# Performance work log

Measured on AMD Instinct MI355X. Metric: run time of the kernel, lower is better.

The kernel has to match this reference:

```python
import jax, jax.numpy as jnp
import numpy as np

N, E, G = 50000, 800000, 128
IN, HID, OUT, H = 128, 64, 32, 4
EPS = 1e-5


def _bn(x, g, b, m, v):
    # BatchNorm1d in eval mode: normalize with running stats
    return (x - m) * jax.lax.rsqrt(v + EPS) * g + b


def _gat(x, src, dst, W, att_src, att_dst, bias, n):
    # PyG GATConv, concat=False: mean over heads
    h = (x @ W).reshape(n, H, -1)                      # [N,H,C]
    a_src = (h * att_src).sum(-1)                      # [N,H]
    a_dst = (h * att_dst).sum(-1)                      # [N,H]
    e = jax.nn.leaky_relu(a_src[src] + a_dst[dst], 0.2)  # [E,H]
    m = jax.ops.segment_max(e, dst, num_segments=n)    # segment softmax over incoming edges
    e = jnp.exp(e - m[dst])
    s = jax.ops.segment_sum(e, dst, num_segments=n)
    alpha = e / s[dst]                                  # [E,H]
    out = jax.ops.segment_sum(alpha[:, :, None] * h[src], dst, num_segments=n)  # [N,H,C]
    return out.mean(axis=1) + bias


def setup_inputs() -> dict:
    key = jax.random.key(0)
    ks = jax.random.split(key, 20)
    d = {
        "x": jax.random.normal(ks[0], (N, IN), jnp.float32),
        "edge_index": jax.random.randint(ks[1], (2, E), 0, N),
        "batch": jnp.sort(jax.random.randint(ks[2], (N,), 0, G)),
        # input_norm
        "in_gamma": jax.random.normal(ks[3], (IN,)) * 0.05 + 1.0,
        "in_beta": jax.random.normal(ks[4], (IN,)) * 0.05,
        "in_mean": jax.random.normal(ks[5], (IN,)) * 0.05,
        "in_var": jax.random.uniform(ks[6], (IN,)) + 0.5,
        # gat1
        "W1": jax.random.normal(ks[7], (IN, H * HID)) * (1.0 / np.sqrt(IN)),
        "as1": jax.random.normal(ks[8], (H, HID)) * 0.1,
        "ad1": jax.random.normal(ks[9], (H, HID)) * 0.1,
        "b1": jnp.zeros((HID,)),
        "bn1_g": jnp.ones((HID,)),
        "bn1_b": jnp.zeros((HID,)),
        "bn1_m": jax.random.normal(ks[10], (HID,)) * 0.05,
        "bn1_v": jax.random.uniform(ks[11], (HID,)) + 0.5,
        # gat2
        "W2": jax.random.normal(ks[12], (HID, H * HID)) * (1.0 / np.sqrt(HID)),
        "as2": jax.random.normal(ks[13], (H, HID)) * 0.1,
        "ad2": jax.random.normal(ks[14], (H, HID)) * 0.1,
        "b2": jnp.zeros((HID,)),
        "bn2_g": jnp.ones((HID,)),
        "bn2_b": jnp.zeros((HID,)),
        "bn2_m": jax.random.normal(ks[15], (HID,)) * 0.05,
        "bn2_v": jax.random.uniform(ks[16], (HID,)) + 0.5,
        # head
        "fc1_w": jax.random.normal(ks[17], (HID, HID // 2)) * (1.0 / np.sqrt(HID)),
        "fc1_b": jnp.zeros((HID // 2,)),
        "fc2_w": jax.random.normal(ks[18], (HID // 2, OUT)) * (1.0 / np.sqrt(HID // 2)),
        "fc2_b": jnp.zeros((OUT,)),
    }
    return d


def reference(x, edge_index, batch, in_gamma, in_beta, in_mean, in_var,
              W1, as1, ad1, b1, bn1_g, bn1_b, bn1_m, bn1_v,
              W2, as2, ad2, b2, bn2_g, bn2_b, bn2_m, bn2_v,
              fc1_w, fc1_b, fc2_w, fc2_b):
    n = x.shape[0]
    # PyG GATConv adds self-loops by default
    loop = jnp.arange(n)
    src = jnp.concatenate([edge_index[0], loop])
    dst = jnp.concatenate([edge_index[1], loop])

    h = _bn(x, in_gamma, in_beta, in_mean, in_var)
    h = _gat(h, src, dst, W1, as1, ad1, b1, n)
    h = jax.nn.relu(_bn(h, bn1_g, bn1_b, bn1_m, bn1_v))
    # dropout p=0.3 is identity in eval mode
    h = _gat(h, src, dst, W2, as2, ad2, b2, n)
    h = jax.nn.relu(_bn(h, bn2_g, bn2_b, bn2_m, bn2_v))

    # global mean pool over graphs
    sums = jax.ops.segment_sum(h, batch, num_segments=G)
    cnts = jax.ops.segment_sum(jnp.ones((n,), h.dtype), batch, num_segments=G)
    emb = sums / jnp.maximum(cnts, 1.0)[:, None]

    out = jax.nn.relu(emb @ fc1_w + fc1_b)
    return out @ fc2_w + fc2_b
```

## Files before the change

### kernel.cpp

```cpp
#include <hip/hip_runtime.h>
#include <hip/hip_bf16.h>

#define EPS   1e-5f
#define NH    4
#define DIN   128
#define DHID  64
#define DOUT  32
#define PNODES 256
#define CAP   128
#define GM    32
#define NBUCK 64
#define BSTR  16
#define EPT   16
#define EPB   (256 * EPT)

typedef __attribute__((ext_vector_type(8))) short short8;
typedef __attribute__((ext_vector_type(4))) float f32x4;
typedef __attribute__((ext_vector_type(2))) float f32x2;

__device__ __forceinline__ float us2f(unsigned short u) {
    return __uint_as_float((unsigned)u << 16);
}
__device__ __forceinline__ unsigned short f2us(float v) {
    __hip_bfloat16 hb = __float2bfloat16(v);
    return *(unsigned short*)&hb;
}
__device__ __forceinline__ unsigned char f2e4m3(float v) {
    int p = __builtin_amdgcn_cvt_pk_fp8_f32(v, 0.f, 0, false);
    return (unsigned char)(p & 0xff);
}
__device__ __forceinline__ float lrelu(float a) { return (a >= 0.f) ? a : 0.2f * a; }

__global__ __launch_bounds__(256) void k_setup(
    int* __restrict__ deg, float* __restrict__ pool, int* __restrict__ bcur,
    int N, int npool,
    const float* __restrict__ ing, const float* __restrict__ inb,
    const float* __restrict__ inm, const float* __restrict__ inv,
    const float* __restrict__ W1, const float* __restrict__ W2,
    const float* __restrict__ as1, const float* __restrict__ ad1,
    const float* __restrict__ as2, const float* __restrict__ ad2,
    const float* __restrict__ b1,
    const float* __restrict__ bn1g, const float* __restrict__ bn1b,
    const float* __restrict__ bn1m, const float* __restrict__ bn1v,
    unsigned short* __restrict__ Wt, unsigned short* __restrict__ Wt2,
    unsigned short* __restrict__ Wast1, unsigned short* __restrict__ Wast2,
    float* __restrict__ scl1, float* __restrict__ shf1,
    float* __restrict__ sclX, float* __restrict__ shfX)
{
    int g = blockIdx.x * blockDim.x + threadIdx.x;
    if (g < N) deg[g] = 1;
    if (g < npool) pool[g] = 0.f;
    if (g < NBUCK * BSTR) bcur[g] = 0;
    if (g < 256 * DIN) {
        int n = g >> 7, k = g & 127;
        Wt[g] = f2us(W1[(size_t)k * 256 + n]);
    }
    if (g < 256 * DHID) {
        int n = g >> 6, k = g & 63;
        Wt2[g] = f2us(W2[(size_t)k * 256 + n]);
    }
    if (g < 16 * DIN) {
        int c = g >> 7, k = g & 127;
        float s = 0.f;
        if (c < 4)      { for (int j = 0; j < 64; ++j) s += W1[(size_t)k * 256 + c * 64 + j] * as1[c * 64 + j]; }
        else if (c < 8) { for (int j = 0; j < 64; ++j) s += W1[(size_t)k * 256 + (c - 4) * 64 + j] * ad1[(c - 4) * 64 + j]; }
        Wast1[g] = f2us(s);
    }
    if (g < 16 * DHID) {
        int c = g >> 6, k = g & 63;
        float s = 0.f;
        if (c < 4)      { for (int j = 0; j < 64; ++j) s += W2[(size_t)k * 256 + c * 64 + j] * as2[c * 64 + j]; }
        else if (c < 8) { for (int j = 0; j < 64; ++j) s += W2[(size_t)k * 256 + (c - 4) * 64 + j] * ad2[(c - 4) * 64 + j]; }
        Wast2[g] = f2us(s);
    }
    if (g < DHID) {
        float sc = bn1g[g] * rsqrtf(bn1v[g] + EPS);
        scl1[g] = sc;
        shf1[g] = (b1[g] - bn1m[g]) * sc + bn1b[g];
    }
    if (g < DIN) {
        float sc = ing[g] * rsqrtf(inv[g] + EPS);
        sclX[g] = sc;
        shfX[g] = inb[g] - inm[g] * sc;
    }
}

__global__ __launch_bounds__(256) void k_scan_a(const int* __restrict__ deg,
                                                int* __restrict__ rowptr,
                                                int* __restrict__ bsum, int N) {
    __shared__ int sh[256];
    const int t = threadIdx.x;
    const int i = blockIdx.x * 256 + t;
    int v = (i < N) ? deg[i] : 0;
    sh[t] = v;
    __syncthreads();
    #pragma unroll
    for (int o = 1; o < 256; o <<= 1) {
        int u = (t >= o) ? sh[t - o] : 0;
        __syncthreads();
        sh[t] += u;
        __syncthreads();
    }
    if (i < N) rowptr[i] = sh[t] - v;
    if (t == 255) bsum[blockIdx.x] = sh[255];
}

__global__ __launch_bounds__(256) void k_scan_c2(int* __restrict__ rowptr,
                                                 int* __restrict__ cursor,
                                                 const int* __restrict__ bsum,
                                                 int N, int Etot, int nb) {
    __shared__ int sh[256];
    const int t = threadIdx.x;
    int v = (t < nb) ? bsum[t] : 0;
    sh[t] = v;
    __syncthreads();
    #pragma unroll
    for (int o = 1; o < 256; o <<= 1) {
        int u = (t >= o) ? sh[t - o] : 0;
        __syncthreads();
        sh[t] += u;
        __syncthreads();
    }
    const int off = (blockIdx.x > 0) ? sh[blockIdx.x - 1] : 0;
    const int i = blockIdx.x * 256 + t;
    if (i < N) {
        int r = rowptr[i] + off;
        rowptr[i] = r;
        cursor[i] = r;
    }
    if (i == 0) rowptr[N] = Etot;
}

__global__ __launch_bounds__(256) void k_part(
    const int* __restrict__ ei, int E, int N, int bshift,
    unsigned long long* __restrict__ arena, int* __restrict__ bcur,
    int* __restrict__ deg, int cap)
{
    __shared__ int lhist[NBUCK];
    __shared__ int lbase[NBUCK];
    const int t = threadIdx.x;
    const int e0 = blockIdx.x * EPB;
    const int eEnd = min(e0 + EPB, E + N);

    if (t < NBUCK) lhist[t] = 0;
    __syncthreads();

    int myb[EPT], myd[EPT], mys[EPT];
    #pragma unroll
    for (int r = 0; r < EPT; ++r) {
        int e = e0 + r * 256 + t;
        myb[r] = -1;
        if (e < eEnd) {
            int s, d;
            if (e < E) { s = ei[e]; d = ei[E + e]; atomicAdd(&deg[d], 1); }
            else       { s = d = e - E; }
            int b = d >> bshift;
            myb[r] = b; myd[r] = d; mys[r] = s;
            atomicAdd(&lhist[b], 1);
        }
    }
    __syncthreads();

    if (t < NBUCK) {
        int c = lhist[t];
        lbase[t] = c ? atomicAdd(&bcur[t * BSTR], c) : 0;
        lhist[t] = 0;
    }
    __syncthreads();

    #pragma unroll
    for (int r = 0; r < EPT; ++r) {
        int b = myb[r];
        if (b >= 0) {
            int li = atomicAdd(&lhist[b], 1);
            int pos = lbase[b] + li;
            if (pos >= cap) pos = cap - 1;
            arena[(size_t)b * cap + pos] =
                ((unsigned long long)(unsigned)myd[r] << 32) | (unsigned)mys[r];
        }
    }
}

__global__ __launch_bounds__(256) void k_fill2(
    const unsigned long long* __restrict__ arena, const int* __restrict__ bcur,
    int cap, int* __restrict__ cursor, int* __restrict__ col)
{
    const int b = blockIdx.x;
    const int idx = blockIdx.y * 256 + threadIdx.x;
    if (idx >= bcur[b * BSTR]) return;
    unsigned long long v = arena[(size_t)b * cap + idx];
    int d = (int)(v >> 32);
    int s = (int)(v & 0xffffffffu);
    int pos = atomicAdd(&cursor[d], 1);
    col[pos] = s;
}

__global__ __launch_bounds__(256) void k_gemm1(
    const float* __restrict__ x,
    const float* __restrict__ sclX, const float* __restrict__ shfX,
    const unsigned short* __restrict__ Wt,
    const unsigned short* __restrict__ Wast,
    unsigned char* __restrict__ h,
    float* __restrict__ asrc, float* __restrict__ adst, int N)
{
    __shared__ float Csh[GM][260];
    const int t = threadIdx.x;
    const int lane = t & 63, wv = t >> 6;
    const int qm = lane & 15, qd = lane >> 4;
    const int base = blockIdx.x * GM;

    short8 afr[2][4];
    #pragma unroll
    for (int ks = 0; ks < 4; ++ks) {
        const int k0 = qd * 8 + ks * 32;
        float4 s0 = *(const float4*)(sclX + k0), s1 = *(const float4*)(sclX + k0 + 4);
        float4 h0 = *(const float4*)(shfX + k0), h1 = *(const float4*)(shfX + k0 + 4);
        #pragma unroll
        for (int rt = 0; rt < 2; ++rt) {
            int node = base + rt * 16 + qm;
            if (node >= N) node = N - 1;
            const float* xp = x + (size_t)node * DIN + k0;
            float4 x0 = *(const float4*)xp, x1 = *(const float4*)(xp + 4);
            short8 v;
            v[0] = f2us(x0.x * s0.x + h0.x); v[1] = f2us(x0.y * s0.y + h0.y);
            v[2] = f2us(x0.z * s0.z + h0.z); v[3] = f2us(x0.w * s0.w + h0.w);
            v[4] = f2us(x1.x * s1.x + h1.x); v[5] = f2us(x1.y * s1.y + h1.y);
            v[6] = f2us(x1.z * s1.z + h1.z); v[7] = f2us(x1.w * s1.w + h1.w);
            afr[rt][ks] = v;
        }
    }

    const int n0 = wv * 64;
    f32x4 acc[2][4];
    #pragma unroll
    for (int rt = 0; rt < 2; ++rt)
        #pragma unroll
        for (int ct = 0; ct < 4; ++ct)
            acc[rt][ct] = (f32x4){0.f, 0.f, 0.f, 0.f};

    #pragma unroll
    for (int ct = 0; ct < 4; ++ct) {
        const unsigned short* bp = Wt + (size_t)(n0 + ct * 16 + qm) * DIN + qd * 8;
        #pragma unroll
        for (int ks = 0; ks < 4; ++ks) {
            short8 bfr = *(const short8*)(bp + ks * 32);
            acc[0][ct] = __builtin_amdgcn_mfma_f32_16x16x32_bf16(afr[0][ks], bfr, acc[0][ct], 0, 0, 0);
            acc[1][ct] = __builtin_amdgcn_mfma_f32_16x16x32_bf16(afr[1][ks], bfr, acc[1][ct], 0, 0, 0);
        }
    }

    {
        const unsigned short* wp = Wast + (size_t)qm * DIN + qd * 8;
        f32x4 aat[2];
        aat[0] = (f32x4){0.f, 0.f, 0.f, 0.f};
        aat[1] = (f32x4){0.f, 0.f, 0.f, 0.f};
        #pragma unroll
        for (int ks = 0; ks < 4; ++ks) {
            short8 wfr = *(const short8*)(wp + ks * 32);
            aat[0] = __builtin_amdgcn_mfma_f32_16x16x32_bf16(afr[0][ks], wfr, aat[0], 0, 0, 0);
            aat[1] = __builtin_amdgcn_mfma_f32_16x16x32_bf16(afr[1][ks], wfr, aat[1], 0, 0, 0);
        }
        const int c = qm;
        #pragma unroll
        for (int rt = 0; rt < 2; ++rt)
            #pragma unroll
            for (int rg = 0; rg < 4; ++rg) {
                int nd = base + rt * 16 + qd * 4 + rg;
                if (nd < N) {
                    if (c < 4)      asrc[nd * 4 + c] = aat[rt][rg];
                    else if (c < 8) adst[nd * 4 + (c - 4)] = aat[rt][rg];
                }
            }
    }

    #pragma unroll
    for (int rt = 0; rt < 2; ++rt)
        #pragma unroll
        for (int ct = 0; ct < 4; ++ct)
            #pragma unroll
            for (int rg = 0; rg < 4; ++rg)
                Csh[rt * 16 + qd * 4 + rg][n0 + ct * 16 + qm] = acc[rt][ct][rg];
    __syncthreads();

    const int hcol = ((t & 3) << 6) | (t >> 2);
    for (int r = 0; r < GM; ++r) {
        int node = base + r;
        if (node >= N) break;
        h[(size_t)node * 256 + t] = f2e4m3(Csh[r][hcol]);
    }
}

__global__ __launch_bounds__(256) void k_gemm2(
    const unsigned short* __restrict__ A2,
    const unsigned short* __restrict__ Wt2,
    const unsigned short* __restrict__ Wast,
    unsigned char* __restrict__ h,
    float* __restrict__ asrc, float* __restrict__ adst, int N)
{
    __shared__ float Csh[GM][260];
    const int t = threadIdx.x;
    const int lane = t & 63, wv = t >> 6;
    const int qm = lane & 15, qd = lane >> 4;
    const int base = blockIdx.x * GM;

    short8 afr[2][2];
    #pragma unroll
    for (int rt = 0; rt < 2; ++rt) {
        int node = base + rt * 16 + qm;
        if (node >= N) node = N - 1;
        const unsigned short* ap = A2 + (size_t)node * DHID + qd * 8;
        #pragma unroll
        for (int ks = 0; ks < 2; ++ks)
            afr[rt][ks] = *(const short8*)(ap + ks * 32);
    }

    const int n0 = wv * 64;
    f32x4 acc[2][4];
    #pragma unroll
    for (int rt = 0; rt < 2; ++rt)
        #pragma unroll
        for (int ct = 0; ct < 4; ++ct)
            acc[rt][ct] = (f32x4){0.f, 0.f, 0.f, 0.f};

    #pragma unroll
    for (int ct = 0; ct < 4; ++ct) {
        const unsigned short* bp = Wt2 + (size_t)(n0 + ct * 16 + qm) * DHID + qd * 8;
        #pragma unroll
        for (int ks = 0; ks < 2; ++ks) {
            short8 bfr = *(const short8*)(bp + ks * 32);
            acc[0][ct] = __builtin_amdgcn_mfma_f32_16x16x32_bf16(afr[0][ks], bfr, acc[0][ct], 0, 0, 0);
            acc[1][ct] = __builtin_amdgcn_mfma_f32_16x16x32_bf16(afr[1][ks], bfr, acc[1][ct], 0, 0, 0);
        }
    }

    {
        const unsigned short* wp = Wast + (size_t)qm * DHID + qd * 8;
        f32x4 aat[2];
        aat[0] = (f32x4){0.f, 0.f, 0.f, 0.f};
        aat[1] = (f32x4){0.f, 0.f, 0.f, 0.f};
        #pragma unroll
        for (int ks = 0; ks < 2; ++ks) {
            short8 wfr = *(const short8*)(wp + ks * 32);
            aat[0] = __builtin_amdgcn_mfma_f32_16x16x32_bf16(afr[0][ks], wfr, aat[0], 0, 0, 0);
            aat[1] = __builtin_amdgcn_mfma_f32_16x16x32_bf16(afr[1][ks], wfr, aat[1], 0, 0, 0);
        }
        const int c = qm;
        #pragma unroll
        for (int rt = 0; rt < 2; ++rt)
            #pragma unroll
            for (int rg = 0; rg < 4; ++rg) {
                int nd = base + rt * 16 + qd * 4 + rg;
                if (nd < N) {
                    if (c < 4)      asrc[nd * 4 + c] = aat[rt][rg];
                    else if (c < 8) adst[nd * 4 + (c - 4)] = aat[rt][rg];
                }
            }
    }

    #pragma unroll
    for (int rt = 0; rt < 2; ++rt)
        #pragma unroll
        for (int ct = 0; ct < 4; ++ct)
            #pragma unroll
            for (int rg = 0; rg < 4; ++rg)
                Csh[rt * 16 + qd * 4 + rg][n0 + ct * 16 + qm] = acc[rt][ct][rg];
    __syncthreads();

    const int hcol = ((t & 3) << 6) | (t >> 2);
    for (int r = 0; r < GM; ++r) {
        int node = base + r;
        if (node >= N) break;
        h[(size_t)node * 256 + t] = f2e4m3(Csh[r][hcol]);
    }
}

__global__ __launch_bounds__(256) void k_agg(
    const int* __restrict__ rowptr, const int* __restrict__ col,
    const float* __restrict__ asrc, const float* __restrict__ adst,
    const unsigned char* __restrict__ h8,
    float* __restrict__ outf, unsigned short* __restrict__ outb,
    const float* __restrict__ scl, const float* __restrict__ shf,
    int mode, int N)
{
    __shared__ float4 exs[4][CAP];
    __shared__ int    cols[4][CAP];
    const int lane = threadIdx.x & 63;
    const int wv   = threadIdx.x >> 6;
    const int d = (blockIdx.x << 2) + wv;
    if (d >= N) return;
    const int r0  = rowptr[d];
    const int deg = rowptr[d + 1] - r0;

    const float4 ad4 = ((const float4*)adst)[d];
    const float4* __restrict__ as4 = (const float4*)asrc;

    float sm0 = 0.f, sm1 = 0.f, sm2 = 0.f, sm3 = 0.f;
    for (int j = lane; j < deg; j += 64) {
        int s = col[r0 + j];
        float4 a = as4[s];
        float e0 = __expf(lrelu(a.x + ad4.x));
        float e1 = __expf(lrelu(a.y + ad4.y));
        float e2 = __expf(lrelu(a.z + ad4.z));
        float e3 = __expf(lrelu(a.w + ad4.w));
        if (j < CAP) { cols[wv][j] = s; exs[wv][j] = make_float4(e0, e1, e2, e3); }
        sm0 += e0; sm1 += e1; sm2 += e2; sm3 += e3;
    }
    #pragma unroll
    for (int o = 1; o < 64; o <<= 1) {
        sm0 += __shfl_xor(sm0, o, 64);
        sm1 += __shfl_xor(sm1, o, 64);
        sm2 += __shfl_xor(sm2, o, 64);
        sm3 += __shfl_xor(sm3, o, 64);
    }
    const float i0 = 0.25f / sm0, i1 = 0.25f / sm1, i2 = 0.25f / sm2, i3 = 0.25f / sm3;

    const unsigned int* __restrict__ hu = (const unsigned int*)h8;
    float a0 = 0.f, a1 = 0.f, a2 = 0.f, a3 = 0.f;
    float b0 = 0.f, b1 = 0.f, b2 = 0.f, b3 = 0.f;
    if (deg <= CAP) {
        int j = 0;
        for (; j + 3 < deg; j += 4) {
            int sA = cols[wv][j],     sB = cols[wv][j + 1];
            int sC = cols[wv][j + 2], sD = cols[wv][j + 3];
            unsigned int vA = hu[(size_t)sA * 64 + lane];
            unsigned int vB = hu[(size_t)sB * 64 + lane];
            unsigned int vC = hu[(size_t)sC * 64 + lane];
            unsigned int vD = hu[(size_t)sD * 64 + lane];
            float4 wA = exs[wv][j],     wB = exs[wv][j + 1];
            float4 wC = exs[wv][j + 2], wD = exs[wv][j + 3];
            f32x2 lA = __builtin_amdgcn_cvt_pk_f32_fp8(vA, false), hA = __builtin_amdgcn_cvt_pk_f32_fp8(vA, true);
            f32x2 lB = __builtin_amdgcn_cvt_pk_f32_fp8(vB, false), hB = __builtin_amdgcn_cvt_pk_f32_fp8(vB, true);
            f32x2 lC = __builtin_amdgcn_cvt_pk_f32_fp8(vC, false), hC = __builtin_amdgcn_cvt_pk_f32_fp8(vC, true);
            f32x2 lD = __builtin_amdgcn_cvt_pk_f32_fp8(vD, false), hD = __builtin_amdgcn_cvt_pk_f32_fp8(vD, true);
            a0 += wA.x * lA.x; a1 += wA.y * lA.y; a2 += wA.z * hA.x; a3 += wA.w * hA.y;
            b0 += wB.x * lB.x; b1 += wB.y * lB.y; b2 += wB.z * hB.x; b3 += wB.w * hB.y;
            a0 += wC.x * lC.x; a1 += wC.y * lC.y; a2 += wC.z * hC.x; a3 += wC.w * hC.y;
            b0 += wD.x * lD.x; b1 += wD.y * lD.y; b2 += wD.z * hD.x; b3 += wD.w * hD.y;
        }
        for (; j < deg; ++j) {
            int s = cols[wv][j];
            unsigned int v = hu[(size_t)s * 64 + lane];
            float4 w = exs[wv][j];
            f32x2 lo = __builtin_amdgcn_cvt_pk_f32_fp8(v, false), hi = __builtin_amdgcn_cvt_pk_f32_fp8(v, true);
            a0 += w.x * lo.x; a1 += w.y * lo.y; a2 += w.z * hi.x; a3 += w.w * hi.y;
        }
    } else {
        for (int j = 0; j < deg; ++j) {
            int s; float4 w;
            if (j < CAP) { s = cols[wv][j]; w = exs[wv][j]; }
            else {
                s = col[r0 + j];
                float4 a = as4[s];
                w.x = __expf(lrelu(a.x + ad4.x)); w.y = __expf(lrelu(a.y + ad4.y));
                w.z = __expf(lrelu(a.z + ad4.z)); w.w = __expf(lrelu(a.w + ad4.w));
            }
            unsigned int v = hu[(size_t)s * 64 + lane];
            f32x2 lo = __builtin_amdgcn_cvt_pk_f32_fp8(v, false), hi = __builtin_amdgcn_cvt_pk_f32_fp8(v, true);
            a0 += w.x * lo.x; a1 += w.y * lo.y; a2 += w.z * hi.x; a3 += w.w * hi.y;
        }
    }
    float acc = (a0 + b0) * i0 + (a1 + b1) * i1 + (a2 + b2) * i2 + (a3 + b3) * i3;

    if (mode) {
        float v = fmaxf(acc * scl[lane] + shf[lane], 0.f);
        outb[(size_t)d * 64 + lane] = f2us(v);
    } else {
        outf[(size_t)d * 64 + lane] = acc;
    }
}

__global__ __launch_bounds__(256) void k_pool(
    const float* __restrict__ outacc,
    const float* __restrict__ b2_,
    const float* __restrict__ bg, const float* __restrict__ bb,
    const float* __restrict__ bm, const float* __restrict__ bv,
    const int* __restrict__ batch,
    float* __restrict__ pool, float* __restrict__ cnt, int N)
{
    const int lane = threadIdx.x & 63;
    const int wave = threadIdx.x >> 6;
    const int base = blockIdx.x * PNODES;
    int end = base + PNODES; if (end > N) end = N;

    const float scale = bg[lane] * rsqrtf(bv[lane] + EPS);
    const float shift = (b2_[lane] - bm[lane]) * scale + bb[lane];

    float acc = 0.f;
    int cur = -1, cl = 0;
    for (int n = base + wave; n < end; n += 4) {
        int gr = batch[n];
        if (gr != cur) {
            if (cur >= 0) {
                atomicAdd(&pool[cur * 64 + lane], acc);
                if (lane == 0) atomicAdd(&cnt[cur], (float)cl);
            }
            cur = gr; acc = 0.f; cl = 0;
        }
        float v = fmaxf(outacc[(size_t)n * 64 + lane] * scale + shift, 0.f);
        acc += v; ++cl;
    }
    if (cur >= 0) {
        atomicAdd(&pool[cur * 64 + lane], acc);
        if (lane == 0) atomicAdd(&cnt[cur], (float)cl);
    }
}

__global__ void k_head(const float* __restrict__ pool, const float* __restrict__ cnt,
                       const float* __restrict__ fc1w, const float* __restrict__ fc1b,
                       const float* __restrict__ fc2w, const float* __restrict__ fc2b,
                       float* __restrict__ out)
{
    int g = blockIdx.x;
    int t = threadIdx.x;
    __shared__ float emb[64];
    __shared__ float z1[32];
    float c = fmaxf(cnt[g], 1.0f);
    emb[t] = pool[g * 64 + t] / c;
    __syncthreads();
    if (t < 32) {
        float s = fc1b[t];
        for (int k = 0; k < 64; ++k) s += emb[k] * fc1w[k * 32 + t];
        z1[t] = fmaxf(s, 0.f);
    }
    __syncthreads();
    if (t < 32) {
        float o = fc2b[t];
        for (int j = 0; j < 32; ++j) o += z1[j] * fc2w[j * 32 + t];
        out[g * 32 + t] = o;
    }
}

extern "C" void kernel_launch(void* const* d_in, const int* in_sizes, int n_in,
                              void* d_out, int out_size, void* d_ws, size_t ws_size,
                              hipStream_t stream)
{
    const float* x    = (const float*)d_in[0];
    const int*   ei   = (const int*)d_in[1];
    const int*   batch= (const int*)d_in[2];
    const float* ing  = (const float*)d_in[3];
    const float* inb  = (const float*)d_in[4];
    const float* inm  = (const float*)d_in[5];
    const float* inv  = (const float*)d_in[6];
    const float* W1   = (const float*)d_in[7];
    const float* as1  = (const float*)d_in[8];
    const float* ad1  = (const float*)d_in[9];
    const float* b1   = (const float*)d_in[10];
    const float* bn1g = (const float*)d_in[11];
    const float* bn1b = (const float*)d_in[12];
    const float* bn1m = (const float*)d_in[13];
    const float* bn1v = (const float*)d_in[14];
    const float* W2   = (const float*)d_in[15];
    const float* as2  = (const float*)d_in[16];
    const float* ad2  = (const float*)d_in[17];
    const float* b2   = (const float*)d_in[18];
    const float* bn2g = (const float*)d_in[19];
    const float* bn2b = (const float*)d_in[20];
    const float* bn2m = (const float*)d_in[21];
    const float* bn2v = (const float*)d_in[22];
    const float* fc1w = (const float*)d_in[23];
    const float* fc1b = (const float*)d_in[24];
    const float* fc2w = (const float*)d_in[25];
    const float* fc2b = (const float*)d_in[26];

    const int N = in_sizes[0] / DIN;
    const int E = in_sizes[1] / 2;
    const int G = out_size / DOUT;
    const int Etot = E + N;

    int bshift = 0;
    while ((N >> bshift) >= NBUCK) ++bshift;
    const int cap = (int)(((long long)Etot << bshift) / N * 5 / 4) + 512;

    unsigned char* h8 = (unsigned char*)d_ws;
    float* asrc   = (float*)(h8 + (size_t)N * 256);
    float* adst   = asrc + (size_t)N * NH;
    unsigned short* Wt    = (unsigned short*)(adst + (size_t)N * NH);
    unsigned short* Wt2   = Wt + 256 * DIN;
    unsigned short* Wast1 = Wt2 + 256 * DHID;
    unsigned short* Wast2 = Wast1 + 16 * DIN;
    float* scl1   = (float*)(Wast2 + 16 * DHID);
    float* shf1   = scl1 + DHID;
    float* sclX   = shf1 + DHID;
    float* shfX   = sclX + DIN;
    float* outacc = shfX + DIN;
    unsigned short* A2 = (unsigned short*)outacc;
    int*   deg    = (int*)(outacc + (size_t)N * DHID);
    int*   rowptr = deg + N;
    int*   cursor = rowptr + N + 1;
    int*   col    = cursor + N;
    float* pool   = (float*)(col + Etot);
    float* cnt    = pool + (size_t)G * DHID;
    int*   bsum   = (int*)(cnt + G);
    int*   bcur   = (int*)(((size_t)(bsum + 256) + 63) & ~(size_t)63);
    unsigned long long* arena =
        (unsigned long long*)(((size_t)(bcur + NBUCK * BSTR) + 7) & ~(size_t)7);

    const int npool = G * DHID + G;
    const int nScanBlk = (N + 255) / 256;
    dim3 b256(256);

    int setupTot = N;
    if (setupTot < npool) setupTot = npool;
    if (setupTot < 256 * DIN) setupTot = 256 * DIN;
    k_setup<<<(setupTot + 255) / 256, b256, 0, stream>>>(
        deg, pool, bcur, N, npool,
        ing, inb, inm, inv, W1, W2, as1, ad1, as2, ad2,
        b1, bn1g, bn1b, bn1m, bn1v,
        Wt, Wt2, Wast1, Wast2, scl1, shf1, sclX, shfX);

    k_part<<<(Etot + EPB - 1) / EPB, b256, 0, stream>>>(ei, E, N, bshift, arena, bcur, deg, cap);
    k_scan_a<<<nScanBlk, b256, 0, stream>>>(deg, rowptr, bsum, N);
    k_scan_c2<<<nScanBlk, b256, 0, stream>>>(rowptr, cursor, bsum, N, Etot, nScanBlk);
    {
        dim3 gFill(NBUCK, (cap + 255) / 256);
        k_fill2<<<gFill, b256, 0, stream>>>(arena, bcur, cap, cursor, col);
    }

    k_gemm1<<<(N + GM - 1) / GM, b256, 0, stream>>>(x, sclX, shfX, Wt, Wast1, h8, asrc, adst, N);
    k_agg<<<(N + 3) / 4, b256, 0, stream>>>(rowptr, col, asrc, adst, h8,
                                            (float*)nullptr, A2, scl1, shf1, 1, N);

    k_gemm2<<<(N + GM - 1) / GM, b256, 0, stream>>>(A2, Wt2, Wast2, h8, asrc, adst, N);
    k_agg<<<(N + 3) / 4, b256, 0, stream>>>(rowptr, col, asrc, adst, h8,
                                            outacc, (unsigned short*)nullptr,
                                            (const float*)nullptr, (const float*)nullptr, 0, N);

    k_pool<<<(N + PNODES - 1) / PNODES, b256, 0, stream>>>(outacc, b2, bn2g, bn2b, bn2m, bn2v,
                                                           batch, pool, cnt, N);
    k_head<<<G, 64, 0, stream>>>(pool, cnt, fc1w, fc1b, fc2w, fc2b, (float*)d_out);
}
```

Before: 363.9 us.

## Fuse BN2, ReLU and mean-pool into second aggregation; pack accumulators

The standalone pooling kernel is removed. The second aggregation pass now applies the precomputed BN2 scale and shift plus ReLU, then atomically adds each node's row into its graph's pool slot. Per-graph node counts move into the edge-partition kernel, and the aggregation accumulators use packed two-float vectors so the compiler can emit packed FMAs. This avoids writing and re-reading the full float node-feature buffer and saves one launch. The cost is one float atomic per node per channel, all landing on a small set of pool addresses because batch is sorted, so contention is a risk.

After: 522.7 us. +43.7%, slower.

```diff
diff --git a/kernel.cpp b/kernel.cpp
--- a/kernel.cpp
+++ b/kernel.cpp
@@ -6,7 +6,6 @@
 #define DIN   128
 #define DHID  64
 #define DOUT  32
-#define PNODES 256
 #define CAP   128
 #define GM    32
 #define NBUCK 64
@@ -42,9 +41,13 @@
     const float* __restrict__ b1,
     const float* __restrict__ bn1g, const float* __restrict__ bn1b,
     const float* __restrict__ bn1m, const float* __restrict__ bn1v,
+    const float* __restrict__ b2,
+    const float* __restrict__ bn2g, const float* __restrict__ bn2b,
+    const float* __restrict__ bn2m, const float* __restrict__ bn2v,
     unsigned short* __restrict__ Wt, unsigned short* __restrict__ Wt2,
     unsigned short* __restrict__ Wast1, unsigned short* __restrict__ Wast2,
     float* __restrict__ scl1, float* __restrict__ shf1,
+    float* __restrict__ scl2, float* __restrict__ shf2,
     float* __restrict__ sclX, float* __restrict__ shfX)
 {
     int g = blockIdx.x * blockDim.x + threadIdx.x;
@@ -77,6 +80,9 @@
         float sc = bn1g[g] * rsqrtf(bn1v[g] + EPS);
         scl1[g] = sc;
         shf1[g] = (b1[g] - bn1m[g]) * sc + bn1b[g];
+        float sc2 = bn2g[g] * rsqrtf(bn2v[g] + EPS);
+        scl2[g] = sc2;
+        shf2[g] = (b2[g] - bn2m[g]) * sc2 + bn2b[g];
     }
     if (g < DIN) {
         float sc = ing[g] * rsqrtf(inv[g] + EPS);
@@ -134,7 +140,8 @@
 __global__ __launch_bounds__(256) void k_part(
     const int* __restrict__ ei, int E, int N, int bshift,
     unsigned long long* __restrict__ arena, int* __restrict__ bcur,
-    int* __restrict__ deg, int cap)
+    int* __restrict__ deg, int cap,
+    const int* __restrict__ batch, float* __restrict__ cnt)
 {
     __shared__ int lhist[NBUCK];
     __shared__ int lbase[NBUCK];
@@ -153,7 +160,10 @@
         if (e < eEnd) {
             int s, d;
             if (e < E) { s = ei[e]; d = ei[E + e]; atomicAdd(&deg[d], 1); }
-            else       { s = d = e - E; }
+            else {
+                s = d = e - E;
+                atomicAdd(&cnt[batch[s]], 1.f);
+            }
             int b = d >> bshift;
             myb[r] = b; myd[r] = d; mys[r] = s;
             atomicAdd(&lhist[b], 1);
@@ -378,7 +388,8 @@
     const int* __restrict__ rowptr, const int* __restrict__ col,
     const float* __restrict__ asrc, const float* __restrict__ adst,
     const unsigned char* __restrict__ h8,
-    float* __restrict__ outf, unsigned short* __restrict__ outb,
+    float* __restrict__ pool, unsigned short* __restrict__ outb,
+    const int* __restrict__ batch,
     const float* __restrict__ scl, const float* __restrict__ shf,
     int mode, int N)
 {
@@ -415,8 +426,8 @@
     const float i0 = 0.25f / sm0, i1 = 0.25f / sm1, i2 = 0.25f / sm2, i3 = 0.25f / sm3;
 
     const unsigned int* __restrict__ hu = (const unsigned int*)h8;
-    float a0 = 0.f, a1 = 0.f, a2 = 0.f, a3 = 0.f;
-    float b0 = 0.f, b1 = 0.f, b2 = 0.f, b3 = 0.f;
+    f32x2 accA01 = {0.f, 0.f}, accA23 = {0.f, 0.f};
+    f32x2 accB01 = {0.f, 0.f}, accB23 = {0.f, 0.f};
     if (deg <= CAP) {
         int j = 0;
         for (; j + 3 < deg; j += 4) {
@@ -432,17 +443,17 @@
             f32x2 lB = __builtin_amdgcn_cvt_pk_f32_fp8(vB, false), hB = __builtin_amdgcn_cvt_pk_f32_fp8(vB, true);
             f32x2 lC = __builtin_amdgcn_cvt_pk_f32_fp8(vC, false), hC = __builtin_amdgcn_cvt_pk_f32_fp8(vC, true);
             f32x2 lD = __builtin_amdgcn_cvt_pk_f32_fp8(vD, false), hD = __builtin_amdgcn_cvt_pk_f32_fp8(vD, true);
-            a0 += wA.x * lA.x; a1 += wA.y * lA.y; a2 += wA.z * hA.x; a3 += wA.w * hA.y;
-            b0 += wB.x * lB.x; b1 += wB.y * lB.y; b2 += wB.z * hB.x; b3 += wB.w * hB.y;
-            a0 += wC.x * lC.x; a1 += wC.y * lC.y; a2 += wC.z * hC.x; a3 += wC.w * hC.y;
-            b0 += wD.x * lD.x; b1 += wD.y * lD.y; b2 += wD.z * hD.x; b3 += wD.w * hD.y;
+            accA01 += (f32x2){wA.x, wA.y} * lA; accA23 += (f32x2){wA.z, wA.w} * hA;
+            accB01 += (f32x2){wB.x, wB.y} * lB; accB23 += (f32x2){wB.z, wB.w} * hB;
+            accA01 += (f32x2){wC.x, wC.y} * lC; accA23 += (f32x2){wC.z, wC.w} * hC;
+            accB01 += (f32x2){wD.x, wD.y} * lD; accB23 += (f32x2){wD.z, wD.w} * hD;
         }
         for (; j < deg; ++j) {
             int s = cols[wv][j];
             unsigned int v = hu[(size_t)s * 64 + lane];
             float4 w = exs[wv][j];
             f32x2 lo = __builtin_amdgcn_cvt_pk_f32_fp8(v, false), hi = __builtin_amdgcn_cvt_pk_f32_fp8(v, true);
-            a0 += w.x * lo.x; a1 += w.y * lo.y; a2 += w.z * hi.x; a3 += w.w * hi.y;
+            accA01 += (f32x2){w.x, w.y} * lo; accA23 += (f32x2){w.z, w.w} * hi;
         }
     } else {
         for (int j = 0; j < deg; ++j) {
@@ -456,52 +467,20 @@
             }
             unsigned int v = hu[(size_t)s * 64 + lane];
             f32x2 lo = __builtin_amdgcn_cvt_pk_f32_fp8(v, false), hi = __builtin_amdgcn_cvt_pk_f32_fp8(v, true);
-            a0 += w.x * lo.x; a1 += w.y * lo.y; a2 += w.z * hi.x; a3 += w.w * hi.y;
-        }
-    }
-    float acc = (a0 + b0) * i0 + (a1 + b1) * i1 + (a2 + b2) * i2 + (a3 + b3) * i3;
+            accA01 += (f32x2){w.x, w.y} * lo; accA23 += (f32x2){w.z, w.w} * hi;
+        }
+    }
+    f32x2 s01 = accA01 + accB01;
+    f32x2 s23 = accA23 + accB23;
+    float acc = s01.x * i0 + s01.y * i1 + s23.x * i2 + s23.y * i3;
 
     if (mode) {
         float v = fmaxf(acc * scl[lane] + shf[lane], 0.f);
         outb[(size_t)d * 64 + lane] = f2us(v);
     } else {
-        outf[(size_t)d * 64 + lane] = acc;
-    }
-}
-
-__global__ __launch_bounds__(256) void k_pool(
-    const float* __restrict__ outacc,
-    const float* __restrict__ b2_,
-    const float* __restrict__ bg, const float* __restrict__ bb,
-    const float* __restrict__ bm, const float* __restrict__ bv,
-    const int* __restrict__ batch,
-    float* __restrict__ pool, float* __restrict__ cnt, int N)
-{
-    const int lane = threadIdx.x & 63;
-    const int wave = threadIdx.x >> 6;
-    const int base = blockIdx.x * PNODES;
-    int end = base + PNODES; if (end > N) end = N;
-
-    const float scale = bg[lane] * rsqrtf(bv[lane] + EPS);
-    const float shift = (b2_[lane] - bm[lane]) * scale + bb[lane];
-
-    float acc = 0.f;
-    int cur = -1, cl = 0;
-    for (int n = base + wave; n < end; n += 4) {
-        int gr = batch[n];
-        if (gr != cur) {
-            if (cur >= 0) {
-                atomicAdd(&pool[cur * 64 + lane], acc);
-                if (lane == 0) atomicAdd(&cnt[cur], (float)cl);
-            }
-            cur = gr; acc = 0.f; cl = 0;
-        }
-        float v = fmaxf(outacc[(size_t)n * 64 + lane] * scale + shift, 0.f);
-        acc += v; ++cl;
-    }
-    if (cur >= 0) {
-        atomicAdd(&pool[cur * 64 + lane], acc);
-        if (lane == 0) atomicAdd(&cnt[cur], (float)cl);
+        int gr = batch[d];
+        float v = fmaxf(acc * scl[lane] + shf[lane], 0.f);
+        atomicAdd(&pool[(size_t)gr * 64 + lane], v);
     }
 }
 
@@ -580,7 +559,9 @@
     unsigned short* Wast2 = Wast1 + 16 * DIN;
     float* scl1   = (float*)(Wast2 + 16 * DHID);
     float* shf1   = scl1 + DHID;
-    float* sclX   = shf1 + DHID;
+    float* scl2   = shf1 + DHID;
+    float* shf2   = scl2 + DHID;
+    float* sclX   = shf2 + DHID;
     float* shfX   = sclX + DIN;
     float* outacc = shfX + DIN;
     unsigned short* A2 = (unsigned short*)outacc;
@@ -606,9 +587,11 @@
         deg, pool, bcur, N, npool,
         ing, inb, inm, inv, W1, W2, as1, ad1, as2, ad2,
         b1, bn1g, bn1b, bn1m, bn1v,
-        Wt, Wt2, Wast1, Wast2, scl1, shf1, sclX, shfX);
-
-    k_part<<<(Etot + EPB - 1) / EPB, b256, 0, stream>>>(ei, E, N, bshift, arena, bcur, deg, cap);
+        b2, bn2g, bn2b, bn2m, bn2v,
+        Wt, Wt2, Wast1, Wast2, scl1, shf1, scl2, shf2, sclX, shfX);
+
+    k_part<<<(Etot + EPB - 1) / EPB, b256, 0, stream>>>(ei, E, N, bshift, arena, bcur, deg, cap,
+                                                        batch, cnt);
     k_scan_a<<<nScanBlk, b256, 0, stream>>>(deg, rowptr, bsum, N);
     k_scan_c2<<<nScanBlk, b256, 0, stream>>>(rowptr, cursor, bsum, N, Etot, nScanBlk);
     {
@@ -618,14 +601,13 @@
 
     k_gemm1<<<(N + GM - 1) / GM, b256, 0, stream>>>(x, sclX, shfX, Wt, Wast1, h8, asrc, adst, N);
     k_agg<<<(N + 3) / 4, b256, 0, stream>>>(rowptr, col, asrc, adst, h8,
-                                            (float*)nullptr, A2, scl1, shf1, 1, N);
+                                            (float*)nullptr, A2, (const int*)nullptr,
+                                            scl1, shf1, 1, N);
 
     k_gemm2<<<(N + GM - 1) / GM, b256, 0, stream>>>(A2, Wt2, Wast2, h8, asrc, adst, N);
     k_agg<<<(N + 3) / 4, b256, 0, stream>>>(rowptr, col, asrc, adst, h8,
-                                            outacc, (unsigned short*)nullptr,
-                                            (const float*)nullptr, (const float*)nullptr, 0, N);
-
-    k_pool<<<(N + PNODES - 1) / PNODES, b256, 0, stream>>>(outacc, b2, bn2g, bn2b, bn2m, bn2v,
-                                                           batch, pool, cnt, N);
+                                            pool, (unsigned short*)nullptr, batch,
+                                            scl2, shf2, 0, N);
+
     k_head<<<G, 64, 0, stream>>>(pool, cnt, fc1w, fc1b, fc2w, fc2b, (float*)d_out);
 }
```
